# Kernel optimization log

Hardware: AMD Instinct MI355X
Metric: run time of the kernel (lower is better)

The kernel has to match this reference:

```python
import jax, jax.numpy as jnp
import numpy as np

B, S, E = 2, 2048, 2048
N_HEAD = 16
HEAD_DIM = E // N_HEAD  # 128
MP_NUM = 4              # hardcoded in the torch forward
ROTARY_DIM = 64


def setup_inputs() -> dict:
    key = jax.random.key(0)
    k1, k2, k3 = jax.random.split(key, 3)
    return {
        "hidden_states": jax.random.normal(k1, (B, S, E), jnp.float32) * 0.02,
        "w_qkv": jax.random.normal(k2, (3 * E, E), jnp.float32) * 0.02,  # torch Linear weight [out,in]
        "w_out": jax.random.normal(k3, (E, E), jnp.float32) * 0.02,
    }


def _rotate_every_two(x):
    # (..., d) -> interleaved (-x2, x1) as in GPT-J/CodeGen
    x1 = x[..., 0::2]
    x2 = x[..., 1::2]
    return jnp.stack((-x2, x1), axis=-1).reshape(x.shape)


def reference(hidden_states, w_qkv, w_out):
    b, s, e = hidden_states.shape
    local = e // MP_NUM  # per-mp-shard channel count

    # qkv projection (no bias), then mp_num split: order is (query, value, key)
    qkv = jnp.einsum("bse,fe->bsf", hidden_states, w_qkv)  # [B,S,3E]
    qkv = qkv.reshape(b, s, MP_NUM, 3 * local)
    q = qkv[..., :local].reshape(b, s, N_HEAD, HEAD_DIM)
    v = qkv[..., local:2 * local].reshape(b, s, N_HEAD, HEAD_DIM)
    k = qkv[..., 2 * local:].reshape(b, s, N_HEAD, HEAD_DIM)

    # partial rotary (rotate-every-two) on first ROTARY_DIM channels
    inv_freq = 1.0 / (10000.0 ** (jnp.arange(0, ROTARY_DIM, 2, dtype=jnp.float32) / ROTARY_DIM))
    freqs = jnp.arange(s, dtype=jnp.float32)[:, None] * inv_freq[None, :]  # [S, R/2]
    sin = jnp.repeat(jnp.sin(freqs), 2, axis=-1)[None, :, None, :]  # [1,S,1,R]
    cos = jnp.repeat(jnp.cos(freqs), 2, axis=-1)[None, :, None, :]

    def rope(x):
        x_rot = x[..., :ROTARY_DIM]
        x_pass = x[..., ROTARY_DIM:]
        x_rot = x_rot * cos + _rotate_every_two(x_rot) * sin
        return jnp.concatenate([x_rot, x_pass], axis=-1)

    q = rope(q)
    k = rope(k)

    # [B,S,H,D] -> [B,H,S,D]
    q = q.transpose(0, 2, 1, 3)
    k = k.transpose(0, 2, 1, 3)
    v = v.transpose(0, 2, 1, 3)

    scale = jnp.sqrt(jnp.asarray(HEAD_DIM, dtype=q.dtype))
    scores = jnp.einsum("bhqd,bhkd->bhqk", q, k) / scale  # [B,H,S,S]
    causal = jnp.tril(jnp.ones((s, s), dtype=bool))
    scores = jnp.where(causal[None, None, :, :], scores, jnp.finfo(scores.dtype).min)
    attn = jax.nn.softmax(scores, axis=-1)

    out = jnp.einsum("bhqk,bhkd->bhqd", attn, v)  # [B,H,S,D]
    out = out.transpose(0, 2, 1, 3).reshape(b, s, e)  # merge heads
    return jnp.einsum("bse,fe->bsf", out, w_out)  # out_proj (no bias)
```

## Files before the change

### kernel.cpp

```cpp
#include <hip/hip_runtime.h>

typedef unsigned short u16;
typedef unsigned int u32;
typedef __attribute__((ext_vector_type(4))) float f32x4;
typedef __attribute__((ext_vector_type(8))) short s16x8;
typedef __attribute__((ext_vector_type(4))) unsigned int u32x4;

#define DEVI static __device__ __forceinline__


#define ROPE_C (-13.287712379549449f / 32.0f)
#define QSCALE 0.12751743f

DEVI u16 f2bf(float f) {
  u32 u = __float_as_uint(f);
  return (u16)((u + 0x7FFFu + ((u >> 16) & 1u)) >> 16);
}
DEVI float bf2f(u16 h) { return __uint_as_float(((u32)h) << 16); }

DEVI void async_copy16(const u16* g, u16* l) {
  __builtin_amdgcn_global_load_lds((__attribute__((address_space(1))) void*)g,
                                   (__attribute__((address_space(3))) void*)l, 16, 0, 0);
}

__global__ __launch_bounds__(256) void cast3_kernel(
    const float* __restrict__ s0, u16* __restrict__ d0, int n0,
    const float* __restrict__ s1, u16* __restrict__ d1, int n1,
    const float* __restrict__ s2, u16* __restrict__ d2, int n2) {
  int i = blockIdx.x * 256 + threadIdx.x;
  const float* s;
  u16* d;
  if (i < n0) {
    s = s0; d = d0;
  } else if (i < n0 + n1) {
    s = s1; d = d1; i -= n0;
  } else if (i < n0 + n1 + n2) {
    s = s2; d = d2; i -= n0 + n1;
  } else {
    return;
  }
  const float4 v = ((const float4*)s)[i];
  ushort4 o;
  o.x = f2bf(v.x); o.y = f2bf(v.y); o.z = f2bf(v.z); o.w = f2bf(v.w);
  ((ushort4*)d)[i] = o;
}

template <int EPI>
__global__ __launch_bounds__(256, 3) void gemm_bt_kernel(
    const u16* __restrict__ A, const u16* __restrict__ Bm, int K, int N,
    float* __restrict__ C, u16* __restrict__ qo, u16* __restrict__ ko, u16* __restrict__ vo) {
  __shared__ __attribute__((aligned(16))) u16 As[3][128 * 32];
  __shared__ __attribute__((aligned(16))) u16 Bs[3][128 * 32];
  const int tid = threadIdx.x;
  const int w = tid >> 6, lane = tid & 63;
  const int quad = lane >> 4, l16 = lane & 15;
  const int wrow = (w >> 1) * 64, wcol = (w & 1) * 64;
  const long tileM = (long)blockIdx.y * 128;
  const long tileN = (long)blockIdx.x * 128;

  f32x4 acc[4][4];
#pragma unroll
  for (int i = 0; i < 4; ++i)
#pragma unroll
    for (int j = 0; j < 4; ++j) acc[i][j] = f32x4{0.f, 0.f, 0.f, 0.f};

  const u16* aptr[2];
  const u16* bptr[2];
  int ldso[2];
#pragma unroll
  for (int c = 0; c < 2; ++c) {
    const int r0 = (w * 2 + c) * 16;
    const int row = r0 + (lane >> 2);
    const int colsw = (((lane & 3) ^ ((row >> 1) & 3)) << 3);
    aptr[c] = A + (tileM + row) * (long)K + colsw;
    bptr[c] = Bm + (tileN + row) * (long)K + colsw;
    ldso[c] = r0 * 32;
  }

  auto stage = [&](int k0, int buf) {
#pragma unroll
    for (int c = 0; c < 2; ++c) {
      async_copy16(aptr[c] + k0, &As[buf][ldso[c]]);
      async_copy16(bptr[c] + k0, &Bs[buf][ldso[c]]);
    }
  };

  stage(0, 0);
  stage(32, 1);

  const int psw = (quad ^ ((l16 >> 1) & 3)) << 3;

  int bt = 0;
  for (int k0 = 0; k0 < K; k0 += 32) {
    if (k0 + 32 < K)
      __builtin_amdgcn_s_waitcnt(0x0f74);
    else
      __builtin_amdgcn_s_waitcnt(0x0f70);
    __builtin_amdgcn_s_barrier();
    if (k0 + 64 < K) stage(k0 + 64, bt == 0 ? 2 : bt - 1);

    s16x8 af[4], bfr[4];
#pragma unroll
    for (int i = 0; i < 4; ++i)
      af[i] = *(const s16x8*)(&As[bt][(wrow + i * 16 + l16) * 32 + psw]);
#pragma unroll
    for (int j = 0; j < 4; ++j)
      bfr[j] = *(const s16x8*)(&Bs[bt][(wcol + j * 16 + l16) * 32 + psw]);
#pragma unroll
    for (int i = 0; i < 4; ++i)
#pragma unroll
      for (int j = 0; j < 4; ++j)
        acc[i][j] = __builtin_amdgcn_mfma_f32_16x16x32_bf16(af[i], bfr[j], acc[i][j], 0, 0, 0);
    bt = bt == 2 ? 0 : bt + 1;
  }

  const int b = (int)(tileM >> 11);
#pragma unroll
  for (int i = 0; i < 4; ++i) {
#pragma unroll
    for (int j = 0; j < 4; ++j) {
      const int rowb = (int)((tileM + wrow + i * 16 + quad * 4) & 2047);
      if (EPI == 0) {
#pragma unroll
        for (int r = 0; r < 4; ++r) {
          const long row = tileM + wrow + i * 16 + quad * 4 + r;
          C[row * N + tileN + wcol + j * 16 + l16] = acc[i][j][r];
        }
      } else {
        const long col0 = tileN + wcol + j * 16;
        const int mp = (int)(col0 / 1536);
        const int cc0 = (int)(col0 - (long)mp * 1536);
        const int part = cc0 >> 9;
        const int idx0 = cc0 & 511;
        const int head = mp * 4 + (idx0 >> 7);
        const int dim0 = idx0 & 127;
        const int dim = dim0 + l16;
        const long bh = (long)(b * 16 + head);
        if (part == 1) {
#pragma unroll
          for (int r = 0; r < 4; ++r)
            vo[(bh * 128 + dim) * 2048 + rowb + r] = f2bf(acc[i][j][r]);
        } else {
          float y[4];
          if (part == 2 && dim0 < 64) {
            const int jj = dim >> 1;
            const float inv = exp2f((float)jj * ROPE_C);
#pragma unroll
            for (int r = 0; r < 4; ++r) {
              const float v = acc[i][j][r];
              const float pv = __shfl_xor(v, 1, 64);
              const float ang = (float)(rowb + r) * inv;
              const float sn = __sinf(ang), cs = __cosf(ang);
              y[r] = (l16 & 1) ? (v * cs + pv * sn) : (v * cs - pv * sn);
            }
          } else {
#pragma unroll
            for (int r = 0; r < 4; ++r) y[r] = acc[i][j][r];
          }
          u16* dst = (part == 0) ? qo : ko;
#pragma unroll
          for (int r = 0; r < 4; ++r)
            dst[(bh * 2048 + rowb + r) * 128 + dim] = f2bf(y[r]);
        }
      }
    }
  }
}

__global__ __launch_bounds__(256, 4) void attn_kernel(
    const u16* __restrict__ q, const u16* __restrict__ k,
    const u16* __restrict__ vT, u16* __restrict__ out) {
  __shared__ __attribute__((aligned(16))) u16 Ks[2][32 * 128];
  __shared__ __attribute__((aligned(16))) u16 Vs[2][128 * 32];
  const int tid = threadIdx.x;
  const int w = tid >> 6, lane = tid & 63;
  const int quad = lane >> 4, l16 = lane & 15;
  const int qt = 31 - (blockIdx.x >> 5);
  const int bh = blockIdx.x & 31;
  const int qbase = qt * 64 + w * 16;

  const u16* qp = q + ((long)bh * 2048 + qbase) * 128;
  const u16* kp = k + (long)bh * 2048 * 128;
  const u16* vp = vT + (long)bh * 128 * 2048;

  const float spos = (float)(qbase + l16);
  s16x8 qf[4];
#pragma unroll
  for (int c = 0; c < 4; ++c) {
    const s16x8 raw = *(const s16x8*)(qp + l16 * 128 + c * 32 + quad * 8);
    s16x8 ov;
    if (c < 2) {
#pragma unroll
      for (int m = 0; m < 4; ++m) {
        const int jj = c * 16 + quad * 4 + m;
        const float inv = exp2f((float)jj * ROPE_C);
        const float ang = spos * inv;
        const float sn = __sinf(ang), cs = __cosf(ang);
        const float x0 = bf2f((u16)raw[2 * m]), x1 = bf2f((u16)raw[2 * m + 1]);
        ov[2 * m] = (short)f2bf((x0 * cs - x1 * sn) * QSCALE);
        ov[2 * m + 1] = (short)f2bf((x1 * cs + x0 * sn) * QSCALE);
      }
    } else {
#pragma unroll
      for (int e = 0; e < 8; ++e) ov[e] = (short)f2bf(bf2f((u16)raw[e]) * QSCALE);
    }
    qf[c] = ov;
  }

  f32x4 acc[8];
#pragma unroll
  for (int d = 0; d < 8; ++d) acc[d] = f32x4{0.f, 0.f, 0.f, 0.f};
  float mrun = -1e30f, lrun = 0.f;

  auto stage = [&](int k0, int buf) {
    const int ko = lane >> 4, cl = lane & 15;
#pragma unroll
    for (int i = 0; i < 2; ++i) {
      const int keyt = w * 8 + i * 4;
      const int key = keyt + ko;
      async_copy16(kp + (long)(k0 + key) * 128 + ((cl ^ (key & 15)) << 3),
                   &Ks[buf][keyt * 128]);
    }
    const int ld = lane >> 2, c4 = lane & 3;
#pragma unroll
    for (int i = 0; i < 2; ++i) {
      const int db = w * 32 + i * 16;
      const int d = db + ld;
      async_copy16(vp + (long)d * 2048 + k0 + ((c4 ^ ((d >> 1) & 3)) << 3),
                   &Vs[buf][db * 32]);
    }
  };

  stage(0, 0);

  const int nt = 2 * qt + 2;
  for (int t = 0; t < nt; ++t) {
    const int k0 = t * 32;
    const u16* Ksc = Ks[t & 1];
    const u16* Vsc = Vs[t & 1];
    __builtin_amdgcn_s_waitcnt(0x0f70);
    __syncthreads();
    if (t + 1 < nt) stage(k0 + 32, (t + 1) & 1);

    f32x4 sc[2];
#pragma unroll
    for (int g = 0; g < 2; ++g) {
      sc[g] = f32x4{0.f, 0.f, 0.f, 0.f};
#pragma unroll
      for (int c = 0; c < 4; ++c) {
        const s16x8 kf = *(const s16x8*)(
            &Ksc[(g * 16 + l16) * 128 + ((((c << 2) + quad) ^ l16) << 3)]);
        sc[g] = __builtin_amdgcn_mfma_f32_16x16x32_bf16(kf, qf[c], sc[g], 0, 0, 0);
      }
    }
    if (k0 + 31 > qbase) {
      const int qrow = qbase + l16;
#pragma unroll
      for (int g = 0; g < 2; ++g) {
        const int keyb = k0 + g * 16 + quad * 4;
#pragma unroll
        for (int r = 0; r < 4; ++r)
          if (keyb + r > qrow) sc[g][r] = -1e30f;
      }
    }
    float mx = fmaxf(fmaxf(fmaxf(sc[0][0], sc[0][1]), fmaxf(sc[0][2], sc[0][3])),
                     fmaxf(fmaxf(sc[1][0], sc[1][1]), fmaxf(sc[1][2], sc[1][3])));
    mx = fmaxf(mx, __shfl_xor(mx, 16, 64));
    mx = fmaxf(mx, __shfl_xor(mx, 32, 64));
    const float mnew = fmaxf(mrun, mx);
    const float alpha = exp2f(mrun - mnew);
    mrun = mnew;
    float p[2][4];
    float sm = 0.f;
#pragma unroll
    for (int g = 0; g < 2; ++g)
#pragma unroll
      for (int r = 0; r < 4; ++r) { p[g][r] = exp2f(sc[g][r] - mnew); sm += p[g][r]; }
    sm += __shfl_xor(sm, 16, 64);
    sm += __shfl_xor(sm, 32, 64);
    lrun = lrun * alpha + sm;
#pragma unroll
    for (int d = 0; d < 8; ++d)
#pragma unroll
      for (int r = 0; r < 4; ++r) acc[d][r] *= alpha;

    u32 pk[2][2];
#pragma unroll
    for (int g = 0; g < 2; ++g) {
      pk[g][0] = (u32)f2bf(p[g][0]) | ((u32)f2bf(p[g][1]) << 16);
      pk[g][1] = (u32)f2bf(p[g][2]) | ((u32)f2bf(p[g][3]) << 16);
    }
    const int la = ((quad & 1) << 5) + l16;
    const int lb = la + 16;
    const u32 a0 = (u32)__shfl((int)pk[0][0], la, 64);
    const u32 a1 = (u32)__shfl((int)pk[0][1], la, 64);
    const u32 a2 = (u32)__shfl((int)pk[0][0], lb, 64);
    const u32 a3 = (u32)__shfl((int)pk[0][1], lb, 64);
    const u32 b0 = (u32)__shfl((int)pk[1][0], la, 64);
    const u32 b1 = (u32)__shfl((int)pk[1][1], la, 64);
    const u32 b2 = (u32)__shfl((int)pk[1][0], lb, 64);
    const u32 b3 = (u32)__shfl((int)pk[1][1], lb, 64);
    const bool hi = quad >= 2;
    const u32x4 pw = {hi ? b0 : a0, hi ? b1 : a1, hi ? b2 : a2, hi ? b3 : a3};
    const s16x8 pf = __builtin_bit_cast(s16x8, pw);

#pragma unroll
    for (int dd = 0; dd < 8; ++dd) {
      const s16x8 vf = *(const s16x8*)(
          &Vsc[(dd * 16 + l16) * 32 + ((quad ^ ((l16 >> 1) & 3)) << 3)]);
      acc[dd] = __builtin_amdgcn_mfma_f32_16x16x32_bf16(vf, pf, acc[dd], 0, 0, 0);
    }
  }

  const int b = bh >> 4, h = bh & 15;
  u16* op = out + ((long)b * 2048 + qbase + l16) * 2048 + h * 128;
  const float inv_l = 1.0f / lrun;
#pragma unroll
  for (int dd = 0; dd < 8; ++dd) {
    ushort4 o4;
    o4.x = f2bf(acc[dd][0] * inv_l);
    o4.y = f2bf(acc[dd][1] * inv_l);
    o4.z = f2bf(acc[dd][2] * inv_l);
    o4.w = f2bf(acc[dd][3] * inv_l);
    *(ushort4*)(op + dd * 16 + quad * 4) = o4;
  }
}

extern "C" void kernel_launch(void* const* d_in, const int* in_sizes, int n_in,
                              void* d_out, int out_size, void* d_ws, size_t ws_size,
                              hipStream_t stream) {
  const float* hidden = (const float*)d_in[0];
  const float* w_qkv = (const float*)d_in[1];
  const float* w_out = (const float*)d_in[2];
  float* out = (float*)d_out;
  char* ws = (char*)d_ws;

  u16* hid_b  = (u16*)(ws + (size_t)0);
  u16* wqkv_b = (u16*)(ws + (size_t)16777216);
  u16* wout_b = (u16*)(ws + (size_t)41943040);
  u16* qb     = (u16*)(ws + (size_t)50331648);
  u16* kb     = (u16*)(ws + (size_t)67108864);
  u16* vb     = (u16*)(ws + (size_t)83886080);
  u16* ao     = (u16*)(ws + (size_t)100663296);

  cast3_kernel<<<24576, 256, 0, stream>>>(hidden, hid_b, 2097152,
                                          w_qkv, wqkv_b, 3145728,
                                          w_out, wout_b, 1048576);

  gemm_bt_kernel<1><<<dim3(48, 32), 256, 0, stream>>>(hid_b, wqkv_b, 2048, 6144,
                                                      nullptr, qb, kb, vb);
  attn_kernel<<<1024, 256, 0, stream>>>(qb, kb, vb, ao);
  gemm_bt_kernel<0><<<dim3(16, 32), 256, 0, stream>>>(ao, wout_b, 2048, 2048,
                                                      out, nullptr, nullptr, nullptr);
}
```

Measured before the change: 390.3 us.

## Use 256x256-tile 512-thread GEMM with staged LDS pipeline for QKV projection

Replaces the QKV projection GEMM with a new kernel that uses 256x256 output tiles, 8 waves per block, double-buffered async global-to-LDS loads and a four-phase MFMA schedule that interleaves LDS reads, prefetches and barriers with raised wave priority. Larger tiles raise arithmetic intensity and cut redundant global loads, and the phased schedule aims to overlap memory traffic with matrix math. The grid shrinks to 384 blocks with two blocks per CU allowed, which may underfill 256 CUs, and the larger register and LDS footprint limits occupancy. The epilogue with rotary embedding and head scatter is carried over from the old kernel.

```diff
diff --git a/kernel.cpp b/kernel.cpp
--- a/kernel.cpp
+++ b/kernel.cpp
@@ -167,6 +167,193 @@
   }
 }
 
+__global__ __launch_bounds__(512, 2) void gemm_qkv256_kernel(
+    const u16* __restrict__ A, const u16* __restrict__ Bm, int K,
+    u16* __restrict__ qo, u16* __restrict__ ko, u16* __restrict__ vo) {
+  __shared__ __attribute__((aligned(16))) u16 As[2][2][128 * 64];
+  __shared__ __attribute__((aligned(16))) u16 Bs[2][2][128 * 64];
+  const int tid = threadIdx.x;
+  const int w = tid >> 6, lane = tid & 63;
+  const int quad = lane >> 4, l16 = lane & 15;
+  const int wm = w >> 2, wn = w & 3;
+  const long tileM = (long)blockIdx.y * 256;
+  const long tileN = (long)blockIdx.x * 256;
+
+  f32x4 acc[8][4];
+#pragma unroll
+  for (int i = 0; i < 8; ++i)
+#pragma unroll
+    for (int j = 0; j < 4; ++j) acc[i][j] = f32x4{0.f, 0.f, 0.f, 0.f};
+
+  const int rowoff = lane >> 3;
+  const int swz = ((lane & 7) ^ rowoff) << 3;
+  const u16* aBase = A + (tileM + w * 16 + rowoff) * (long)K + swz;
+  const u16* bBase = Bm + (tileN + w * 16 + rowoff) * (long)K + swz;
+  const int ldsb = (w * 16) * 64;
+
+  auto stageA2 = [&](int t) {
+    const int buf = t & 1;
+    const long k0 = (long)t << 6;
+#pragma unroll
+    for (int h = 0; h < 2; ++h)
+#pragma unroll
+      for (int c = 0; c < 2; ++c)
+        async_copy16(aBase + (long)(h * 128 + c * 8) * K + k0,
+                     &As[buf][h][ldsb + c * 8 * 64]);
+  };
+  auto stageB2 = [&](int t) {
+    const int buf = t & 1;
+    const long k0 = (long)t << 6;
+#pragma unroll
+    for (int h = 0; h < 2; ++h)
+#pragma unroll
+      for (int c = 0; c < 2; ++c)
+        async_copy16(bBase + (long)(h * 128 + c * 8) * K + k0,
+                     &Bs[buf][h][ldsb + c * 8 * 64]);
+  };
+
+  const int gsw = l16 & 7;
+  auto rdA = [&](int buf, int i, int kk) -> s16x8 {
+    return *(const s16x8*)(
+        &As[buf][wm][(i * 16 + l16) * 64 + ((((kk << 2) + quad) ^ gsw) << 3)]);
+  };
+  auto rdB = [&](int buf, int j, int kk) -> s16x8 {
+    return *(const s16x8*)(
+        &Bs[buf][wn >> 1][(((wn & 1) * 64) + j * 16 + l16) * 64 +
+                          ((((kk << 2) + quad) ^ gsw) << 3)]);
+  };
+
+  const int NT = K >> 6;
+  stageB2(0); stageA2(0);
+  stageB2(1); stageA2(1);
+  __builtin_amdgcn_s_waitcnt(0x0f78);
+  __builtin_amdgcn_s_barrier();
+
+  for (int t = 0; t < NT; ++t) {
+    const int buf = t & 1;
+    const bool pf = (t + 2 < NT);
+    s16x8 a[4][2], b0[2][2], b1[2][2];
+
+#pragma unroll
+    for (int i = 0; i < 4; ++i)
+#pragma unroll
+      for (int kk = 0; kk < 2; ++kk) a[i][kk] = rdA(buf, i, kk);
+#pragma unroll
+    for (int j = 0; j < 2; ++j)
+#pragma unroll
+      for (int kk = 0; kk < 2; ++kk) b0[j][kk] = rdB(buf, j, kk);
+    __builtin_amdgcn_s_barrier();
+    __builtin_amdgcn_s_setprio(1);
+#pragma unroll
+    for (int i = 0; i < 4; ++i)
+#pragma unroll
+      for (int j = 0; j < 2; ++j)
+#pragma unroll
+        for (int kk = 0; kk < 2; ++kk)
+          acc[i][j] =
+              __builtin_amdgcn_mfma_f32_16x16x32_bf16(a[i][kk], b0[j][kk], acc[i][j], 0, 0, 0);
+    __builtin_amdgcn_s_setprio(0);
+    __builtin_amdgcn_s_barrier();
+
+#pragma unroll
+    for (int j = 0; j < 2; ++j)
+#pragma unroll
+      for (int kk = 0; kk < 2; ++kk) b1[j][kk] = rdB(buf, 2 + j, kk);
+    __builtin_amdgcn_s_barrier();
+    __builtin_amdgcn_s_setprio(1);
+#pragma unroll
+    for (int i = 0; i < 4; ++i)
+#pragma unroll
+      for (int j = 0; j < 2; ++j)
+#pragma unroll
+        for (int kk = 0; kk < 2; ++kk)
+          acc[i][2 + j] = __builtin_amdgcn_mfma_f32_16x16x32_bf16(a[i][kk], b1[j][kk],
+                                                                  acc[i][2 + j], 0, 0, 0);
+    __builtin_amdgcn_s_setprio(0);
+    __builtin_amdgcn_s_barrier();
+
+    if (pf) stageB2(t + 2);
+#pragma unroll
+    for (int i = 0; i < 4; ++i)
+#pragma unroll
+      for (int kk = 0; kk < 2; ++kk) a[i][kk] = rdA(buf, 4 + i, kk);
+    __builtin_amdgcn_s_barrier();
+    __builtin_amdgcn_s_setprio(1);
+#pragma unroll
+    for (int i = 0; i < 4; ++i)
+#pragma unroll
+      for (int j = 0; j < 2; ++j)
+#pragma unroll
+        for (int kk = 0; kk < 2; ++kk)
+          acc[4 + i][j] = __builtin_amdgcn_mfma_f32_16x16x32_bf16(a[i][kk], b0[j][kk],
+                                                                  acc[4 + i][j], 0, 0, 0);
+    __builtin_amdgcn_s_setprio(0);
+    __builtin_amdgcn_s_barrier();
+
+    if (pf) stageA2(t + 2);
+    __builtin_amdgcn_s_barrier();
+    __builtin_amdgcn_s_setprio(1);
+#pragma unroll
+    for (int i = 0; i < 4; ++i)
+#pragma unroll
+      for (int j = 0; j < 2; ++j)
+#pragma unroll
+        for (int kk = 0; kk < 2; ++kk)
+          acc[4 + i][2 + j] = __builtin_amdgcn_mfma_f32_16x16x32_bf16(
+              a[i][kk], b1[j][kk], acc[4 + i][2 + j], 0, 0, 0);
+    __builtin_amdgcn_s_setprio(0);
+    if (pf)
+      __builtin_amdgcn_s_waitcnt(0x0f78);
+    else
+      __builtin_amdgcn_s_waitcnt(0x0f70);
+    __builtin_amdgcn_s_barrier();
+  }
+
+  const int b = (int)(tileM >> 11);
+#pragma unroll
+  for (int i = 0; i < 8; ++i) {
+#pragma unroll
+    for (int j = 0; j < 4; ++j) {
+      const int rowb = (int)((tileM + wm * 128 + i * 16 + quad * 4) & 2047);
+      const long col0 = tileN + wn * 64 + j * 16;
+      const int mp = (int)(col0 / 1536);
+      const int cc0 = (int)(col0 - (long)mp * 1536);
+      const int part = cc0 >> 9;
+      const int idx0 = cc0 & 511;
+      const int head = mp * 4 + (idx0 >> 7);
+      const int dim0 = idx0 & 127;
+      const int dim = dim0 + l16;
+      const long bh = (long)(b * 16 + head);
+      if (part == 1) {
+#pragma unroll
+        for (int r = 0; r < 4; ++r)
+          vo[(bh * 128 + dim) * 2048 + rowb + r] = f2bf(acc[i][j][r]);
+      } else {
+        float y[4];
+        if (part == 2 && dim0 < 64) {
+          const int jj = dim >> 1;
+          const float inv = exp2f((float)jj * ROPE_C);
+#pragma unroll
+          for (int r = 0; r < 4; ++r) {
+            const float v = acc[i][j][r];
+            const float pv = __shfl_xor(v, 1, 64);
+            const float ang = (float)(rowb + r) * inv;
+            const float sn = __sinf(ang), cs = __cosf(ang);
+            y[r] = (l16 & 1) ? (v * cs + pv * sn) : (v * cs - pv * sn);
+          }
+        } else {
+#pragma unroll
+          for (int r = 0; r < 4; ++r) y[r] = acc[i][j][r];
+        }
+        u16* dst = (part == 0) ? qo : ko;
+#pragma unroll
+        for (int r = 0; r < 4; ++r)
+          dst[(bh * 2048 + rowb + r) * 128 + dim] = f2bf(y[r]);
+      }
+    }
+  }
+}
+
 __global__ __launch_bounds__(256, 4) void attn_kernel(
     const u16* __restrict__ q, const u16* __restrict__ k,
     const u16* __restrict__ vT, u16* __restrict__ out) {
@@ -347,8 +534,8 @@
                                           w_qkv, wqkv_b, 3145728,
                                           w_out, wout_b, 1048576);
 
-  gemm_bt_kernel<1><<<dim3(48, 32), 256, 0, stream>>>(hid_b, wqkv_b, 2048, 6144,
-                                                      nullptr, qb, kb, vb);
+  gemm_qkv256_kernel<<<dim3(24, 16), 512, 0, stream>>>(hid_b, wqkv_b, 2048,
+                                                       qb, kb, vb);
   attn_kernel<<<1024, 256, 0, stream>>>(qb, kb, vb, ao);
   gemm_bt_kernel<0><<<dim3(16, 32), 256, 0, stream>>>(ao, wout_b, 2048, 2048,
                                                       out, nullptr, nullptr, nullptr);
```

Result: slower. 401.8 us (+3.0%).

## Triple-buffer K/V tiles, lazy softmax rescale, and MFMA priority hints in attention

Applied to the files above, without the earlier changes.

The attention kernel moves from double to triple buffering of K/V tiles in LDS, prefetching two tiles ahead and waiting on a partial vmcnt with a plain barrier instead of a full drain plus __syncthreads. The online softmax now rescales the running max and accumulators only when some lane's new max exceeds the old one by more than 8, which skips most rescale multiplies. MFMA sections are wrapped in s_setprio, and the QK loop interleaves its two score groups. The larger LDS footprint lowers the occupancy target from 4 to 3 blocks per CU, and the lazy rescale allows exponent values up to 2^8 before renormalising.

```diff
diff --git a/kernel.cpp b/kernel.cpp
--- a/kernel.cpp
+++ b/kernel.cpp
@@ -167,11 +167,11 @@
   }
 }
 
-__global__ __launch_bounds__(256, 4) void attn_kernel(
+__global__ __launch_bounds__(256, 3) void attn_kernel(
     const u16* __restrict__ q, const u16* __restrict__ k,
     const u16* __restrict__ vT, u16* __restrict__ out) {
-  __shared__ __attribute__((aligned(16))) u16 Ks[2][32 * 128];
-  __shared__ __attribute__((aligned(16))) u16 Vs[2][128 * 32];
+  __shared__ __attribute__((aligned(16))) u16 Ks[3][32 * 128];
+  __shared__ __attribute__((aligned(16))) u16 Vs[3][128 * 32];
   const int tid = threadIdx.x;
   const int w = tid >> 6, lane = tid & 63;
   const int quad = lane >> 4, l16 = lane & 15;
@@ -231,28 +231,36 @@
     }
   };
 
+  const int nt = 2 * qt + 2;
   stage(0, 0);
-
-  const int nt = 2 * qt + 2;
+  stage(32, 1);
+
+  int bt = 0;
   for (int t = 0; t < nt; ++t) {
     const int k0 = t * 32;
-    const u16* Ksc = Ks[t & 1];
-    const u16* Vsc = Vs[t & 1];
-    __builtin_amdgcn_s_waitcnt(0x0f70);
-    __syncthreads();
-    if (t + 1 < nt) stage(k0 + 32, (t + 1) & 1);
+    if (t + 1 < nt)
+      __builtin_amdgcn_s_waitcnt(0x0f74);
+    else
+      __builtin_amdgcn_s_waitcnt(0x0f70);
+    __builtin_amdgcn_s_barrier();
+    if (t + 2 < nt) stage(k0 + 64, bt == 0 ? 2 : bt - 1);
+    const u16* Ksc = Ks[bt];
+    const u16* Vsc = Vs[bt];
 
     f32x4 sc[2];
-#pragma unroll
-    for (int g = 0; g < 2; ++g) {
-      sc[g] = f32x4{0.f, 0.f, 0.f, 0.f};
-#pragma unroll
-      for (int c = 0; c < 4; ++c) {
-        const s16x8 kf = *(const s16x8*)(
-            &Ksc[(g * 16 + l16) * 128 + ((((c << 2) + quad) ^ l16) << 3)]);
-        sc[g] = __builtin_amdgcn_mfma_f32_16x16x32_bf16(kf, qf[c], sc[g], 0, 0, 0);
-      }
-    }
+    sc[0] = f32x4{0.f, 0.f, 0.f, 0.f};
+    sc[1] = f32x4{0.f, 0.f, 0.f, 0.f};
+    __builtin_amdgcn_s_setprio(1);
+#pragma unroll
+    for (int c = 0; c < 4; ++c) {
+      const s16x8 kf0 = *(const s16x8*)(
+          &Ksc[(0 * 16 + l16) * 128 + ((((c << 2) + quad) ^ l16) << 3)]);
+      const s16x8 kf1 = *(const s16x8*)(
+          &Ksc[(1 * 16 + l16) * 128 + ((((c << 2) + quad) ^ l16) << 3)]);
+      sc[0] = __builtin_amdgcn_mfma_f32_16x16x32_bf16(kf0, qf[c], sc[0], 0, 0, 0);
+      sc[1] = __builtin_amdgcn_mfma_f32_16x16x32_bf16(kf1, qf[c], sc[1], 0, 0, 0);
+    }
+    __builtin_amdgcn_s_setprio(0);
     if (k0 + 31 > qbase) {
       const int qrow = qbase + l16;
 #pragma unroll
@@ -267,22 +275,25 @@
                      fmaxf(fmaxf(sc[1][0], sc[1][1]), fmaxf(sc[1][2], sc[1][3])));
     mx = fmaxf(mx, __shfl_xor(mx, 16, 64));
     mx = fmaxf(mx, __shfl_xor(mx, 32, 64));
-    const float mnew = fmaxf(mrun, mx);
-    const float alpha = exp2f(mrun - mnew);
-    mrun = mnew;
+    if (__any(mx > mrun + 8.f)) {
+      const float mnew = fmaxf(mrun, mx);
+      const float alpha = exp2f(mrun - mnew);
+      mrun = mnew;
+      lrun *= alpha;
+#pragma unroll
+      for (int d = 0; d < 8; ++d)
+#pragma unroll
+        for (int r = 0; r < 4; ++r) acc[d][r] *= alpha;
+    }
     float p[2][4];
     float sm = 0.f;
 #pragma unroll
     for (int g = 0; g < 2; ++g)
 #pragma unroll
-      for (int r = 0; r < 4; ++r) { p[g][r] = exp2f(sc[g][r] - mnew); sm += p[g][r]; }
+      for (int r = 0; r < 4; ++r) { p[g][r] = exp2f(sc[g][r] - mrun); sm += p[g][r]; }
     sm += __shfl_xor(sm, 16, 64);
     sm += __shfl_xor(sm, 32, 64);
-    lrun = lrun * alpha + sm;
-#pragma unroll
-    for (int d = 0; d < 8; ++d)
-#pragma unroll
-      for (int r = 0; r < 4; ++r) acc[d][r] *= alpha;
+    lrun += sm;
 
     u32 pk[2][2];
 #pragma unroll
@@ -304,12 +315,15 @@
     const u32x4 pw = {hi ? b0 : a0, hi ? b1 : a1, hi ? b2 : a2, hi ? b3 : a3};
     const s16x8 pf = __builtin_bit_cast(s16x8, pw);
 
+    __builtin_amdgcn_s_setprio(1);
 #pragma unroll
     for (int dd = 0; dd < 8; ++dd) {
       const s16x8 vf = *(const s16x8*)(
           &Vsc[(dd * 16 + l16) * 32 + ((quad ^ ((l16 >> 1) & 3)) << 3)]);
       acc[dd] = __builtin_amdgcn_mfma_f32_16x16x32_bf16(vf, pf, acc[dd], 0, 0, 0);
     }
+    __builtin_amdgcn_s_setprio(0);
+    bt = bt == 2 ? 0 : bt + 1;
   }
 
   const int b = bh >> 4, h = bh & 15;
```

Measured after the change: 383.8 us. About the same (-1.6%).
